# Performance work log

Hardware: AMD Instinct MI355X
Metric: run time of the kernel (lower is better)

The kernel has to match this reference:

```python
import jax, jax.numpy as jnp
import numpy as np

H = 8            # n_heads
CAP = 512        # capacity
TOPK = 2
N_HOPS = 2
ROPE_BASE = 10000.0
VOCAB = 32000
D = 512


def rope_cos_sin(T, dh, base):
    inv = 1.0 / (base ** (jnp.arange(0, dh, 2, dtype=jnp.float32) / dh))
    f = jnp.arange(T, dtype=jnp.float32)[:, None] * inv[None, :]   # [T, dh/2]
    emb = jnp.concatenate([f, f], axis=-1)                          # [T, dh]
    return jnp.cos(emb), jnp.sin(emb)


def rmsnorm(x, s):
    return x * jax.lax.rsqrt(jnp.mean(x * x, axis=-1, keepdims=True) + 1e-6) * s


def rotate_half(x):
    x1, x2 = jnp.split(x, 2, axis=-1)
    return jnp.concatenate([-x2, x1], axis=-1)


def attn_block(x, cos, sin, wqkv, wo, ln_s):
    # pre-norm causal attention with RoPE; residual included (module returns x + attn)
    C, d = x.shape
    dh = d // H
    u = rmsnorm(x, ln_s)
    qkv = u @ wqkv.T                                   # [C, 3d]
    q, k, v = [t.reshape(C, H, dh) for t in jnp.split(qkv, 3, axis=-1)]
    c = cos[:, None, :]; s = sin[:, None, :]
    q = q * c + rotate_half(q) * s
    k = k * c + rotate_half(k) * s
    scores = jnp.einsum('qhd,khd->hqk', q, k) / jnp.sqrt(jnp.float32(dh))
    causal = jnp.tril(jnp.ones((C, C), dtype=bool))
    scores = jnp.where(causal[None], scores, -1e9)
    a = jax.nn.softmax(scores, axis=-1)
    o = jnp.einsum('hqk,khd->qhd', a, v).reshape(C, d)
    return x + o @ wo.T


def ffn_block(x, w1, w2, ln_s):
    u = rmsnorm(x, ln_s)
    return x + jax.nn.gelu(u @ w1.T) @ w2.T


def hop(h, wr, attn_qkv, attn_o, attn_ln, ffn_w1, ffn_w2, ffn_ln, cos, sin):
    T, d = h.shape
    E_total = wr.shape[0]
    E = E_total - 1                                    # last expert = identity
    logits = h @ wr.T                                  # [T, E_total]
    probs = jax.nn.softmax(logits, axis=-1)
    _, idx = jax.lax.top_k(logits, TOPK)
    mask = jax.nn.one_hot(idx, E_total).sum(axis=-2) > 0     # [T, E_total]
    probs_tr = probs[:, :-1]
    mask_tr = mask[:, :-1]
    # capacity select: per-expert top-cap gated tokens -> one-hot slot [E, cap, T]
    g = jnp.where(mask_tr.T, probs_tr.T, -jnp.inf)     # [E, T]
    cap = min(CAP, T)
    _, top_idx = jax.lax.top_k(g, cap)                 # [E, cap]
    slot = jnp.zeros((E, cap, T), jnp.float32).at[
        jnp.arange(E)[:, None], jnp.arange(cap)[None, :], top_idx].set(1.0)
    slot = slot * mask_tr.T[:, None, :]
    kept = slot.sum(axis=1) > 0                        # [E, T]
    # dispatch
    xin = jnp.einsum('ect,td->ecd', slot, h)
    cos_r = jnp.einsum('ect,td->ecd', slot, cos)
    sin_r = jnp.einsum('ect,td->ecd', slot, sin)
    attn_idx = jnp.arange(0, E, 2)
    ffn_idx = jnp.arange(1, E, 2)
    out_a = jax.vmap(attn_block)(xin[attn_idx], cos_r[attn_idx], sin_r[attn_idx],
                                 attn_qkv, attn_o, attn_ln)
    out_f = jax.vmap(ffn_block)(xin[ffn_idx], ffn_w1, ffn_w2, ffn_ln)
    expert_out = jnp.zeros_like(xin).at[attn_idx].set(out_a).at[ffn_idx].set(out_f)
    # combine
    combine_w = jnp.where(kept.T, probs_tr, 0.0)       # [T, E]
    rho = combine_w.sum(axis=-1, keepdims=True)        # [T, 1]
    combine = jnp.einsum('ecd,ect,et->td', expert_out, slot, combine_w.T)
    return h + combine - rho * h


def setup_inputs() -> dict:
    key = jax.random.key(0)
    ks = jax.random.split(key, 12)
    T = 2048
    sc = 0.02
    return {
        'ids': jax.random.randint(ks[0], (T,), 0, VOCAB),
        'embed_w': jax.random.normal(ks[1], (VOCAB, D), jnp.float32) * sc,
        'router_w': jax.random.normal(ks[2], (N_HOPS, 9, D), jnp.float32) * sc,
        'attn_qkv': jax.random.normal(ks[3], (4, 3 * D, D), jnp.float32) * sc,
        'attn_o': jax.random.normal(ks[4], (4, D, D), jnp.float32) * sc,
        'attn_ln': jnp.ones((4, D), jnp.float32),
        'ffn_w1': jax.random.normal(ks[5], (4, 4 * D, D), jnp.float32) * sc,
        'ffn_w2': jax.random.normal(ks[6], (4, D, 4 * D), jnp.float32) * sc,
        'ffn_ln': jnp.ones((4, D), jnp.float32),
        'bb_qkv': jax.random.normal(ks[7], (3 * D, D), jnp.float32) * sc,
        'bb_o': jax.random.normal(ks[8], (D, D), jnp.float32) * sc,
        'bb_ln': jnp.ones((D,), jnp.float32),
        'lnout_s': jnp.ones((D,), jnp.float32),
    }


def reference(ids, embed_w, router_w, attn_qkv, attn_o, attn_ln,
              ffn_w1, ffn_w2, ffn_ln, bb_qkv, bb_o, bb_ln, lnout_s):
    T = ids.shape[0]
    dh = D // H
    h = embed_w[ids]                                   # [T, D]
    cos, sin = rope_cos_sin(T, dh, ROPE_BASE)
    h = attn_block(h, cos, sin, bb_qkv, bb_o, bb_ln)   # backbone (num_backbone=1)
    for i in range(router_w.shape[0]):                 # n_hops routed layers
        h = hop(h, router_w[i], attn_qkv, attn_o, attn_ln,
                ffn_w1, ffn_w2, ffn_ln, cos, sin)
    return rmsnorm(h, lnout_s)
```

## Files before the change

### kernel.cpp

```cpp
#include <hip/hip_runtime.h>
#include <hip/hip_bf16.h>

#define T_SEQ 2048
#define DMODEL 512
#define CEXP 512

typedef short s16x4 __attribute__((ext_vector_type(4)));
typedef short s16x8 __attribute__((ext_vector_type(8)));
typedef float f32x4 __attribute__((ext_vector_type(4)));

__device__ __forceinline__ float geluf(float x){
  float x3 = x*x*x;
  return 0.5f*x*(1.f + tanhf(0.7978845608028654f*(x + 0.044715f*x3)));
}

__device__ __forceinline__ unsigned short f2b(float x){
  unsigned int u = __float_as_uint(x);
  u += 0x7fffu + ((u >> 16) & 1u);
  return (unsigned short)(u >> 16);
}

__global__ void embed_kernel(const int* __restrict__ ids, const float* __restrict__ ew,
                             float* __restrict__ h){
  int idx = blockIdx.x*256 + threadIdx.x;
  int t = idx >> 9, d = idx & 511;
  h[idx] = ew[(size_t)ids[t]*DMODEL + d];
}

__global__ void rope_table_kernel(float* __restrict__ cosb, float* __restrict__ sinb){
  int idx = blockIdx.x*256 + threadIdx.x;
  int t = idx >> 6, i = idx & 63, j = i & 31;
  float inv = powf(10000.f, -(float)(2*j)/64.f);
  float a = (float)t * inv;
  cosb[idx] = cosf(a);
  sinb[idx] = sinf(a);
}

__global__ void rmsnorm_kernel(const float* __restrict__ in, float* __restrict__ out,
                               const float* __restrict__ scale,
                               int rows_per_group, long gstride, int scale_stride){
  int row = blockIdx.x;
  int g = row / rows_per_group, lr = row - g*rows_per_group;
  const float* x = in  + (size_t)g*gstride + (size_t)lr*DMODEL;
  float*       y = out + (size_t)g*gstride + (size_t)lr*DMODEL;
  const float* s = scale + (size_t)g*scale_stride;
  int tid = threadIdx.x;
  float ss = 0.f;
  for (int i = tid; i < DMODEL; i += 256){ float v = x[i]; ss += v*v; }
  __shared__ float red[256];
  red[tid] = ss; __syncthreads();
  for (int st = 128; st > 0; st >>= 1){ if (tid < st) red[tid] += red[tid+st]; __syncthreads(); }
  float r = rsqrtf(red[0]*(1.f/DMODEL) + 1e-6f);
  for (int i = tid; i < DMODEL; i += 256) y[i] = x[i]*r*s[i];
}

__global__ void final_rmsnorm_kernel(const float* __restrict__ in, float* __restrict__ out,
                                     const float* __restrict__ scale){
  int row = blockIdx.x;
  const float* x = in + (size_t)row*DMODEL;
  int tid = threadIdx.x;
  float ss = 0.f;
  for (int i = tid; i < DMODEL; i += 256){ float v = x[i]; ss += v*v; }
  __shared__ float red[256];
  red[tid] = ss; __syncthreads();
  for (int st = 128; st > 0; st >>= 1){ if (tid < st) red[tid] += red[tid+st]; __syncthreads(); }
  float r = rsqrtf(red[0]*(1.f/DMODEL) + 1e-6f);
  for (int i = tid; i < DMODEL; i += 256)
    out[(size_t)row*DMODEL + i] = x[i]*r*scale[i];
}

__global__ __launch_bounds__(256)
void gemm_kernel(const float* __restrict__ A, long Astride,
                 const float* __restrict__ W, long Wstride,
                 const float* __restrict__ Res, long Rstride,
                 float* __restrict__ Out, long Ostride,
                 int M, int N, int K, int act){
  int b = blockIdx.z;
  A += (size_t)b*Astride; W += (size_t)b*Wstride; Out += (size_t)b*Ostride;
  if (Res) Res += (size_t)b*Rstride;
  __shared__ float As[16][68];
  __shared__ float Ws[16][68];
  int tid = threadIdx.x;
  int tx = tid & 15, ty = tid >> 4;
  int row0 = blockIdx.x*64, col0 = blockIdx.y*64;
  float acc[4][4] = {{0.f}};
  int sm = tid >> 2;
  int skq = (tid & 3) << 2;
  int gm = row0 + sm, gn = col0 + sm;

  float4 va = make_float4(0.f,0.f,0.f,0.f);
  float4 vw = make_float4(0.f,0.f,0.f,0.f);
  if (gm < M) va = *(const float4*)&A[(size_t)gm*K + skq];
  if (gn < N) vw = *(const float4*)&W[(size_t)gn*K + skq];

  for (int k0 = 0; k0 < K; k0 += 16){
    __syncthreads();
    As[skq+0][sm] = va.x; As[skq+1][sm] = va.y; As[skq+2][sm] = va.z; As[skq+3][sm] = va.w;
    Ws[skq+0][sm] = vw.x; Ws[skq+1][sm] = vw.y; Ws[skq+2][sm] = vw.z; Ws[skq+3][sm] = vw.w;
    __syncthreads();
    if (k0 + 16 < K){
      if (gm < M) va = *(const float4*)&A[(size_t)gm*K + k0 + 16 + skq];
      if (gn < N) vw = *(const float4*)&W[(size_t)gn*K + k0 + 16 + skq];
    }
    #pragma unroll
    for (int kk = 0; kk < 16; ++kk){
      float4 av = *(const float4*)&As[kk][ty*4];
      float4 wv = *(const float4*)&Ws[kk][tx*4];
      float a[4] = {av.x, av.y, av.z, av.w};
      float w[4] = {wv.x, wv.y, wv.z, wv.w};
      #pragma unroll
      for (int i = 0; i < 4; ++i)
        #pragma unroll
        for (int j = 0; j < 4; ++j)
          acc[i][j] += a[i]*w[j];
    }
  }
  #pragma unroll
  for (int i = 0; i < 4; ++i){
    int om = row0 + ty*4 + i;
    if (om >= M) continue;
    #pragma unroll
    for (int j = 0; j < 4; ++j){
      int on = col0 + tx*4 + j;
      if (on >= N) continue;
      float v = acc[i][j];
      if (act == 1) v = geluf(v);
      if (Res) v += Res[(size_t)om*N + on];
      Out[(size_t)om*N + on] = v;
    }
  }
}

__global__ __launch_bounds__(256)
void gemm128(const float* __restrict__ A, long Astride,
             const float* __restrict__ W, long Wstride,
             const float* __restrict__ Res, long Rstride,
             float* __restrict__ Out, long Ostride,
             int M, int N, int K, int act){
  int b = blockIdx.z;
  A += (size_t)b*Astride; W += (size_t)b*Wstride; Out += (size_t)b*Ostride;
  if (Res) Res += (size_t)b*Rstride;
  __shared__ float As[16][132];
  __shared__ float Ws[16][132];
  int tid = threadIdx.x;
  int r0 = (tid >> 4) * 8;
  int c0 = (tid & 15) * 8;
  int row0 = blockIdx.x*128, col0 = blockIdx.y*128;
  int sr = tid >> 1;
  int sc = (tid & 1) * 8;
  float acc[8][8] = {{0.f}};

  float4 a0 = *(const float4*)&A[(size_t)(row0+sr)*K + sc];
  float4 a1 = *(const float4*)&A[(size_t)(row0+sr)*K + sc + 4];
  float4 w0 = *(const float4*)&W[(size_t)(col0+sr)*K + sc];
  float4 w1 = *(const float4*)&W[(size_t)(col0+sr)*K + sc + 4];

  for (int k0 = 0; k0 < K; k0 += 16){
    __syncthreads();
    As[sc+0][sr]=a0.x; As[sc+1][sr]=a0.y; As[sc+2][sr]=a0.z; As[sc+3][sr]=a0.w;
    As[sc+4][sr]=a1.x; As[sc+5][sr]=a1.y; As[sc+6][sr]=a1.z; As[sc+7][sr]=a1.w;
    Ws[sc+0][sr]=w0.x; Ws[sc+1][sr]=w0.y; Ws[sc+2][sr]=w0.z; Ws[sc+3][sr]=w0.w;
    Ws[sc+4][sr]=w1.x; Ws[sc+5][sr]=w1.y; Ws[sc+6][sr]=w1.z; Ws[sc+7][sr]=w1.w;
    __syncthreads();
    if (k0 + 16 < K){
      a0 = *(const float4*)&A[(size_t)(row0+sr)*K + k0 + 16 + sc];
      a1 = *(const float4*)&A[(size_t)(row0+sr)*K + k0 + 16 + sc + 4];
      w0 = *(const float4*)&W[(size_t)(col0+sr)*K + k0 + 16 + sc];
      w1 = *(const float4*)&W[(size_t)(col0+sr)*K + k0 + 16 + sc + 4];
    }
    #pragma unroll
    for (int kk = 0; kk < 16; ++kk){
      float a[8], w[8];
      *(float4*)&a[0] = *(const float4*)&As[kk][r0];
      *(float4*)&a[4] = *(const float4*)&As[kk][r0+4];
      *(float4*)&w[0] = *(const float4*)&Ws[kk][c0];
      *(float4*)&w[4] = *(const float4*)&Ws[kk][c0+4];
      #pragma unroll
      for (int i = 0; i < 8; ++i)
        #pragma unroll
        for (int j = 0; j < 8; ++j)
          acc[i][j] += a[i]*w[j];
    }
  }

  #pragma unroll
  for (int i = 0; i < 8; ++i){
    int gm = row0 + r0 + i;
    #pragma unroll
    for (int jj = 0; jj < 2; ++jj){
      int gn = col0 + c0 + jj*4;
      float4 v;
      v.x = acc[i][jj*4+0]; v.y = acc[i][jj*4+1];
      v.z = acc[i][jj*4+2]; v.w = acc[i][jj*4+3];
      if (act == 1){ v.x = geluf(v.x); v.y = geluf(v.y); v.z = geluf(v.z); v.w = geluf(v.w); }
      if (Res){
        float4 rv = *(const float4*)&Res[(size_t)gm*N + gn];
        v.x += rv.x; v.y += rv.y; v.z += rv.z; v.w += rv.w;
      }
      *(float4*)&Out[(size_t)gm*N + gn] = v;
    }
  }
}

__global__ __launch_bounds__(256)
void gemm_mfma(const float* __restrict__ A, long Astride,
               const float* __restrict__ W, long Wstride,
               const float* __restrict__ Res, long Rstride,
               float* __restrict__ Out, long Ostride,
               int M, int N, int K, int act){
  int b = blockIdx.z;
  A += (size_t)b*Astride; W += (size_t)b*Wstride; Out += (size_t)b*Ostride;
  if (Res) Res += (size_t)b*Rstride;

  __shared__ short As[128][40];
  __shared__ short Ws[128][40];

  int tid = threadIdx.x;
  int l = tid & 63, w = tid >> 6;
  int wrow = (w >> 1)*64, wcol = (w & 1)*64;
  int row0 = blockIdx.x*128, col0 = blockIdx.y*128;
  int lm = l & 15, lq = l >> 4;

  f32x4 acc[4][4];
  #pragma unroll
  for (int i = 0; i < 4; ++i)
    #pragma unroll
    for (int j = 0; j < 4; ++j)
      acc[i][j] = (f32x4){0.f,0.f,0.f,0.f};

  for (int k0 = 0; k0 < K; k0 += 32){
    #pragma unroll
    for (int t = 0; t < 4; ++t){
      int f4 = tid + t*256;
      int r = f4 >> 3, kq = f4 & 7;
      float4 va = *(const float4*)&A[(size_t)(row0 + r)*K + k0 + kq*4];
      s16x4 pa; pa[0]=(short)f2b(va.x); pa[1]=(short)f2b(va.y); pa[2]=(short)f2b(va.z); pa[3]=(short)f2b(va.w);
      *(s16x4*)&As[r][kq*4] = pa;
      float4 vw = *(const float4*)&W[(size_t)(col0 + r)*K + k0 + kq*4];
      s16x4 pw; pw[0]=(short)f2b(vw.x); pw[1]=(short)f2b(vw.y); pw[2]=(short)f2b(vw.z); pw[3]=(short)f2b(vw.w);
      *(s16x4*)&Ws[r][kq*4] = pw;
    }
    __syncthreads();

    s16x8 af[4], bf[4];
    #pragma unroll
    for (int rt = 0; rt < 4; ++rt)
      af[rt] = *(s16x8*)&As[wrow + rt*16 + lm][lq*8];
    #pragma unroll
    for (int ct = 0; ct < 4; ++ct)
      bf[ct] = *(s16x8*)&Ws[wcol + ct*16 + lm][lq*8];
    #pragma unroll
    for (int rt = 0; rt < 4; ++rt)
      #pragma unroll
      for (int ct = 0; ct < 4; ++ct)
        acc[rt][ct] = __builtin_amdgcn_mfma_f32_16x16x32_bf16(af[rt], bf[ct], acc[rt][ct], 0, 0, 0);
    __syncthreads();
  }

  #pragma unroll
  for (int rt = 0; rt < 4; ++rt){
    #pragma unroll
    for (int p = 0; p < 4; ++p){
      int row = row0 + wrow + rt*16 + lq*4 + p;
      #pragma unroll
      for (int ct = 0; ct < 4; ++ct){
        int col = col0 + wcol + ct*16 + lm;
        float v = acc[rt][ct][p];
        if (act == 1) v = geluf(v);
        if (Res) v += Res[(size_t)row*N + col];
        Out[(size_t)row*N + col] = v;
      }
    }
  }
}

__global__ void rope_kernel(float* __restrict__ qkv, const float* __restrict__ cosb,
                            const float* __restrict__ sinb, const int* __restrict__ map,
                            int map_gstride, int rows_per_group){
  int idx = blockIdx.x*256 + threadIdx.x;
  int row = idx >> 9;
  int rem = idx & 511;
  int sec = rem >> 8;
  int hh  = (rem >> 5) & 7;
  int j   = rem & 31;
  int t;
  if (map){
    t = map[(row/rows_per_group)*map_gstride + (row % rows_per_group)];
    if (t < 0) return;
  } else {
    t = row;
  }
  float c = cosb[t*64 + j], s = sinb[t*64 + j];
  float* p = qkv + (size_t)row*1536 + sec*512 + hh*64;
  float a = p[j], b = p[j+32];
  p[j]    = a*c - b*s;
  p[j+32] = b*c + a*s;
}

__global__ __launch_bounds__(256, 3)
void fattn_kernel(const float* __restrict__ qkv, float* __restrict__ ctx, int C){
  int tps = C >> 4;
  int pairs = tps >> 1;
  int lin = blockIdx.y * gridDim.x + blockIdx.x;
  int hh  = lin & 7;
  int bx  = lin >> 3;
  int seq = bx / pairs;
  int pr  = bx - seq*pairs;
  size_t base = (size_t)seq * C * 1536;
  const float* Qg = qkv + base + hh*64;
  const float* Kg = qkv + base + 512 + hh*64;
  const float* Vg = qkv + base + 1024 + hh*64;

  __shared__ float Qs[16][68];
  __shared__ float Ks[64][68];
  __shared__ float Ps[16][68];

  int tid = threadIdx.x;
  int tx = tid & 15, ty = tid >> 4;

  #pragma unroll 1
  for (int half = 0; half < 2; ++half){
    int lt = half ? pr : (tps - 1 - pr);
    int q0 = lt << 4;
    if (half) __syncthreads();

    *(float4*)&Qs[ty][tx*4] = *(const float4*)&Qg[(size_t)(q0 + ty)*1536 + tx*4];

    float o[4] = {0.f, 0.f, 0.f, 0.f};
    float mrow = -1e30f, lrow = 0.f;

    int nkt = (lt >> 2) + 1;
    for (int kt = 0; kt < nkt; ++kt){
      int k0 = kt << 6;
      if (kt) __syncthreads();
      for (int i = tid; i < 64*16; i += 256){
        int r = i >> 4, dq = i & 15;
        *(float4*)&Ks[r][dq*4] = *(const float4*)&Kg[(size_t)(k0 + r)*1536 + dq*4];
      }
      __syncthreads();

      const float* vbase = Vg + (size_t)k0*1536 + tx*4;
      float4 nv0 = *(const float4*)(vbase + 0*1536);
      float4 nv1 = *(const float4*)(vbase + 1*1536);
      float4 nv2 = *(const float4*)(vbase + 2*1536);
      float4 nv3 = *(const float4*)(vbase + 3*1536);

      float s[4] = {0.f, 0.f, 0.f, 0.f};
      #pragma unroll
      for (int d = 0; d < 64; d += 4){
        float4 qv = *(const float4*)&Qs[ty][d];
        float4 kv[4];
        #pragma unroll
        for (int j = 0; j < 4; ++j) kv[j] = *(const float4*)&Ks[j*16+tx][d];
        #pragma unroll
        for (int j = 0; j < 4; ++j)
          s[j] += qv.x*kv[j].x + qv.y*kv[j].y + qv.z*kv[j].z + qv.w*kv[j].w;
      }
      {
        int q = q0 + ty;
        #pragma unroll
        for (int j = 0; j < 4; ++j){
          int k = k0 + j*16 + tx;
          s[j] = (k <= q) ? s[j]*0.125f : -1e30f;
        }
      }
      {
        float m2 = fmaxf(fmaxf(s[0], s[1]), fmaxf(s[2], s[3]));
        #pragma unroll
        for (int off = 1; off < 16; off <<= 1)
          m2 = fmaxf(m2, __shfl_xor(m2, off, 64));
        float mnew = fmaxf(mrow, m2);
        float alpha = __expf(mrow - mnew);
        float p0 = __expf(s[0] - mnew);
        float p1 = __expf(s[1] - mnew);
        float p2 = __expf(s[2] - mnew);
        float p3 = __expf(s[3] - mnew);
        float rs = (p0 + p1) + (p2 + p3);
        #pragma unroll
        for (int off = 1; off < 16; off <<= 1)
          rs += __shfl_xor(rs, off, 64);
        lrow = lrow*alpha + rs;
        mrow = mnew;
        #pragma unroll
        for (int j = 0; j < 4; ++j) o[j] *= alpha;
        Ps[ty][tx]    = p0;
        Ps[ty][16+tx] = p1;
        Ps[ty][32+tx] = p2;
        Ps[ty][48+tx] = p3;
      }
      {
        #pragma unroll
        for (int kc = 0; kc < 16; ++kc){
          float4 v0 = nv0, v1 = nv1, v2 = nv2, v3 = nv3;
          if (kc < 15){
            const float* nb = vbase + (size_t)(kc+1)*4*1536;
            nv0 = *(const float4*)(nb + 0*1536);
            nv1 = *(const float4*)(nb + 1*1536);
            nv2 = *(const float4*)(nb + 2*1536);
            nv3 = *(const float4*)(nb + 3*1536);
          }
          float4 pr4 = *(const float4*)&Ps[ty][kc*4];
          o[0] += pr4.x*v0.x + pr4.y*v1.x + pr4.z*v2.x + pr4.w*v3.x;
          o[1] += pr4.x*v0.y + pr4.y*v1.y + pr4.z*v2.y + pr4.w*v3.y;
          o[2] += pr4.x*v0.z + pr4.y*v1.z + pr4.z*v2.z + pr4.w*v3.z;
          o[3] += pr4.x*v0.w + pr4.y*v1.w + pr4.z*v2.w + pr4.w*v3.w;
        }
      }
    }

    float inv = 1.f / lrow;
    float4 res;
    res.x = o[0]*inv; res.y = o[1]*inv; res.z = o[2]*inv; res.w = o[3]*inv;
    *(float4*)(ctx + (size_t)(seq*C + q0 + ty)*512 + hh*64 + tx*4) = res;
  }
}

__global__ void router_kernel(const float* __restrict__ logits, float* __restrict__ probs,
                              int* __restrict__ maskb){
  int t = blockIdx.x*256 + threadIdx.x;
  if (t >= T_SEQ) return;
  float v[9];
  float mx = -1e30f;
  for (int e = 0; e < 9; ++e){ v[e] = logits[t*9+e]; mx = fmaxf(mx, v[e]); }
  float s = 0.f;
  for (int e = 0; e < 9; ++e) s += expf(v[e]-mx);
  float inv = 1.f/s;
  for (int e = 0; e < 8; ++e) probs[t*8+e] = expf(v[e]-mx)*inv;
  int i1 = 0;
  for (int e = 1; e < 9; ++e) if (v[e] > v[i1]) i1 = e;
  int i2 = -1;
  for (int e = 0; e < 9; ++e){ if (e == i1) continue; if (i2 < 0 || v[e] > v[i2]) i2 = e; }
  maskb[t] = (1<<i1) | (1<<i2);
}

__global__ void seti_kernel(int* __restrict__ p, int v, int n){
  int i = blockIdx.x*256 + threadIdx.x;
  if (i < n) p[i] = v;
}

__global__ void rank_kernel(const float* __restrict__ probs, const int* __restrict__ maskb,
                            int* __restrict__ t2s, int* __restrict__ s2t, float* __restrict__ cw){
  int idx = blockIdx.x*256 + threadIdx.x;
  int e = idx / T_SEQ, t = idx - e*T_SEQ;
  __shared__ float spm[T_SEQ];
  int tid = threadIdx.x;
  for (int i = tid; i < T_SEQ; i += 256)
    spm[i] = ((maskb[i]>>e)&1) ? probs[i*8+e] : -1.0f;
  __syncthreads();
  int slot = -1; float w = 0.f;
  if ((maskb[t]>>e)&1){
    float p = probs[t*8+e];
    int rank = 0;
    #pragma unroll 8
    for (int t2 = 0; t2 < T_SEQ; ++t2){
      float p2 = spm[t2];
      rank += (p2 > p || (p2 == p && t2 < t)) ? 1 : 0;
    }
    if (rank < CEXP){ slot = rank; w = p; s2t[e*CEXP + rank] = t; }
  }
  t2s[t*8+e] = slot;
  cw[t*8+e] = w;
}

__global__ void gather_kernel(const float* __restrict__ h, const int* __restrict__ s2t,
                              float* __restrict__ xin){
  int idx = blockIdx.x*256 + threadIdx.x;
  int row = idx >> 9, d = idx & 511;
  int t = s2t[row];
  xin[idx] = (t >= 0) ? h[(size_t)t*DMODEL + d] : 0.f;
}

__global__ void combine_kernel(float* __restrict__ h, const float* __restrict__ eout,
                               const int* __restrict__ t2s, const float* __restrict__ cw){
  int idx = blockIdx.x*256 + threadIdx.x;
  int t = idx >> 9, d = idx & 511;
  float acc = 0.f, rho = 0.f;
  for (int e = 0; e < 8; ++e){
    int c = t2s[t*8+e];
    if (c >= 0){
      float w = cw[t*8+e];
      rho += w;
      acc += w * eout[((size_t)e*CEXP + c)*DMODEL + d];
    }
  }
  float hv = h[idx];
  h[idx] = hv + acc - rho*hv;
}

extern "C" void kernel_launch(void* const* d_in, const int* in_sizes, int n_in,
                              void* d_out, int out_size, void* d_ws, size_t ws_size,
                              hipStream_t stream){
  const int*   ids      = (const int*)  d_in[0];
  const float* embed_w  = (const float*)d_in[1];
  const float* router_w = (const float*)d_in[2];
  const float* attn_qkv = (const float*)d_in[3];
  const float* attn_o   = (const float*)d_in[4];
  const float* attn_ln  = (const float*)d_in[5];
  const float* ffn_w1   = (const float*)d_in[6];
  const float* ffn_w2   = (const float*)d_in[7];
  const float* ffn_ln   = (const float*)d_in[8];
  const float* bb_qkv   = (const float*)d_in[9];
  const float* bb_o     = (const float*)d_in[10];
  const float* bb_ln    = (const float*)d_in[11];
  const float* lnout_s  = (const float*)d_in[12];
  float* out = (float*)d_out;

  float* W    = (float*)d_ws;
  float* h    = W;
  float* cosb = h    + 1048576;
  float* sinb = cosb + 131072;
  float* xin  = sinb + 131072;
  float* u    = xin  + 2097152;
  float* big  = u    + 2097152;
  float* ctx  = big  + 4194304;
  float* eout = ctx  + 1048576;
  float* logits = eout + 2097152;
  float* probs  = logits + 18432;
  float* cw     = probs  + 16384;
  int* ibase = (int*)(cw + 16384);
  int* maskb = ibase;
  int* t2s   = maskb + 2048;
  int* s2t   = t2s   + 16384;

  embed_kernel<<<4096, 256, 0, stream>>>(ids, embed_w, h);
  rope_table_kernel<<<512, 256, 0, stream>>>(cosb, sinb);

  rmsnorm_kernel<<<2048, 256, 0, stream>>>(h, u, bb_ln, 2048, 0, 0);
  gemm128<<<dim3(16,12,1), 256, 0, stream>>>(u, 0, bb_qkv, 0, nullptr, 0, big, 0,
                                             2048, 1536, 512, 0);
  rope_kernel<<<4096, 256, 0, stream>>>(big, cosb, sinb, nullptr, 0, 2048);
  fattn_kernel<<<dim3(64,8,1), 256, 0, stream>>>(big, ctx, 2048);
  gemm_kernel<<<dim3(32,8,1), 256, 0, stream>>>(ctx, 0, bb_o, 0, h, 0, h, 0,
                                                2048, 512, 512, 0);

  for (int hop = 0; hop < 2; ++hop){
    const float* wr = router_w + (size_t)hop*9*512;
    gemm_kernel<<<dim3(32,1,1), 256, 0, stream>>>(h, 0, wr, 0, nullptr, 0, logits, 0,
                                                  2048, 9, 512, 0);
    router_kernel<<<8, 256, 0, stream>>>(logits, probs, maskb);
    seti_kernel<<<16, 256, 0, stream>>>(s2t, -1, 4096);
    rank_kernel<<<64, 256, 0, stream>>>(probs, maskb, t2s, s2t, cw);
    gather_kernel<<<8192, 256, 0, stream>>>(h, s2t, xin);

    rmsnorm_kernel<<<2048, 256, 0, stream>>>(xin,          u,          attn_ln, 512, 524288, 512);
    rmsnorm_kernel<<<2048, 256, 0, stream>>>(xin + 262144, u + 262144, ffn_ln,  512, 524288, 512);

    if (hop == 0){
      gemm128<<<dim3(4,12,4), 256, 0, stream>>>(u, 524288, attn_qkv, 786432, nullptr, 0,
                                                big, 786432, 512, 1536, 512, 0);
      rope_kernel<<<4096, 256, 0, stream>>>(big, cosb, sinb, s2t, 1024, 512);
      fattn_kernel<<<dim3(64,8,1), 256, 0, stream>>>(big, ctx, 512);
      gemm_kernel<<<dim3(8,8,4), 256, 0, stream>>>(ctx, 262144, attn_o, 262144,
                                                   xin, 524288, eout, 524288,
                                                   512, 512, 512, 0);
      gemm128<<<dim3(4,16,4), 256, 0, stream>>>(u + 262144, 524288, ffn_w1, 1048576,
                                                nullptr, 0, big, 1048576,
                                                512, 2048, 512, 1);
      gemm_kernel<<<dim3(8,8,4), 256, 0, stream>>>(big, 1048576, ffn_w2, 1048576,
                                                   xin + 262144, 524288, eout + 262144, 524288,
                                                   512, 512, 2048, 0);
    } else {
      gemm_mfma<<<dim3(4,12,4), 256, 0, stream>>>(u, 524288, attn_qkv, 786432, nullptr, 0,
                                                  big, 786432, 512, 1536, 512, 0);
      rope_kernel<<<4096, 256, 0, stream>>>(big, cosb, sinb, s2t, 1024, 512);
      fattn_kernel<<<dim3(64,8,1), 256, 0, stream>>>(big, ctx, 512);
      gemm_mfma<<<dim3(4,4,4), 256, 0, stream>>>(ctx, 262144, attn_o, 262144,
                                                 xin, 524288, eout, 524288,
                                                 512, 512, 512, 0);
      gemm_mfma<<<dim3(4,16,4), 256, 0, stream>>>(u + 262144, 524288, ffn_w1, 1048576,
                                                  nullptr, 0, big, 1048576,
                                                  512, 2048, 512, 1);
      gemm_mfma<<<dim3(4,4,4), 256, 0, stream>>>(big, 1048576, ffn_w2, 1048576,
                                                 xin + 262144, 524288, eout + 262144, 524288,
                                                 512, 512, 2048, 0);
    }

    combine_kernel<<<4096, 256, 0, stream>>>(h, eout, t2s, cw);
  }

  final_rmsnorm_kernel<<<2048, 256, 0, stream>>>(h, out, lnout_s);
}
```

Before: 1.259 ms.

## Merge attention-out and FFN-down GEMMs into one launch; double-buffer K tiles in attention

After: 2.934 ms. 133% more time.

```diff
diff --git a/kernel.cpp b/kernel.cpp
--- a/kernel.cpp
+++ b/kernel.cpp
@@ -19,6 +19,14 @@
   u += 0x7fffu + ((u >> 16) & 1u);
   return (unsigned short)(u >> 16);
 }
+
+struct GP {
+  const float* A; long As;
+  const float* W; long Ws;
+  const float* R; long Rs;
+  float* O; long Os;
+  int M, N, K, act;
+};
 
 __global__ void embed_kernel(const int* __restrict__ ids, const float* __restrict__ ew,
                              float* __restrict__ h){
@@ -69,20 +77,17 @@
     out[(size_t)row*DMODEL + i] = x[i]*r*scale[i];
 }
 
-__global__ __launch_bounds__(256)
-void gemm_kernel(const float* __restrict__ A, long Astride,
-                 const float* __restrict__ W, long Wstride,
-                 const float* __restrict__ Res, long Rstride,
-                 float* __restrict__ Out, long Ostride,
-                 int M, int N, int K, int act){
-  int b = blockIdx.z;
-  A += (size_t)b*Astride; W += (size_t)b*Wstride; Out += (size_t)b*Ostride;
-  if (Res) Res += (size_t)b*Rstride;
+__device__ __forceinline__ void gemm64_body(GP g, int bx, int by, int bz){
+  const float* A = g.A + (size_t)bz*g.As;
+  const float* W = g.W + (size_t)bz*g.Ws;
+  const float* Res = g.R ? g.R + (size_t)bz*g.Rs : nullptr;
+  float* Out = g.O + (size_t)bz*g.Os;
+  int M = g.M, N = g.N, K = g.K, act = g.act;
   __shared__ float As[16][68];
   __shared__ float Ws[16][68];
   int tid = threadIdx.x;
   int tx = tid & 15, ty = tid >> 4;
-  int row0 = blockIdx.x*64, col0 = blockIdx.y*64;
+  int row0 = bx*64, col0 = by*64;
   float acc[4][4] = {{0.f}};
   int sm = tid >> 2;
   int skq = (tid & 3) << 2;
@@ -129,6 +134,17 @@
       Out[(size_t)om*N + on] = v;
     }
   }
+}
+
+__global__ __launch_bounds__(256)
+void gemm_kernel(GP g){ gemm64_body(g, blockIdx.x, blockIdx.y, blockIdx.z); }
+
+__global__ __launch_bounds__(256)
+void gemm_dual(GP g1, GP g2, int ysplit){
+  bool first = (int)blockIdx.y < ysplit;
+  GP g = first ? g1 : g2;
+  int by = first ? blockIdx.y : blockIdx.y - ysplit;
+  gemm64_body(g, blockIdx.x, by, blockIdx.z);
 }
 
 __global__ __launch_bounds__(256)
@@ -202,15 +218,12 @@
   }
 }
 
-__global__ __launch_bounds__(256)
-void gemm_mfma(const float* __restrict__ A, long Astride,
-               const float* __restrict__ W, long Wstride,
-               const float* __restrict__ Res, long Rstride,
-               float* __restrict__ Out, long Ostride,
-               int M, int N, int K, int act){
-  int b = blockIdx.z;
-  A += (size_t)b*Astride; W += (size_t)b*Wstride; Out += (size_t)b*Ostride;
-  if (Res) Res += (size_t)b*Rstride;
+__device__ __forceinline__ void mfma_body(GP g, int bx, int by, int bz){
+  const float* A = g.A + (size_t)bz*g.As;
+  const float* W = g.W + (size_t)bz*g.Ws;
+  const float* Res = g.R ? g.R + (size_t)bz*g.Rs : nullptr;
+  float* Out = g.O + (size_t)bz*g.Os;
+  int N = g.N, K = g.K, act = g.act;
 
   __shared__ short As[128][40];
   __shared__ short Ws[128][40];
@@ -218,7 +231,7 @@
   int tid = threadIdx.x;
   int l = tid & 63, w = tid >> 6;
   int wrow = (w >> 1)*64, wcol = (w & 1)*64;
-  int row0 = blockIdx.x*128, col0 = blockIdx.y*128;
+  int row0 = bx*128, col0 = by*128;
   int lm = l & 15, lq = l >> 4;
 
   f32x4 acc[4][4];
@@ -272,6 +285,17 @@
       }
     }
   }
+}
+
+__global__ __launch_bounds__(256)
+void gemm_mfma(GP g){ mfma_body(g, blockIdx.x, blockIdx.y, blockIdx.z); }
+
+__global__ __launch_bounds__(256)
+void mfma_dual(GP g1, GP g2, int ysplit){
+  bool first = (int)blockIdx.y < ysplit;
+  GP g = first ? g1 : g2;
+  int by = first ? blockIdx.y : blockIdx.y - ysplit;
+  mfma_body(g, blockIdx.x, by, blockIdx.z);
 }
 
 __global__ void rope_kernel(float* __restrict__ qkv, const float* __restrict__ cosb,
@@ -312,11 +336,13 @@
   const float* Vg = qkv + base + 1024 + hh*64;
 
   __shared__ float Qs[16][68];
-  __shared__ float Ks[64][68];
+  __shared__ float Ks[2][64][68];
   __shared__ float Ps[16][68];
 
   int tid = threadIdx.x;
   int tx = tid & 15, ty = tid >> 4;
+  int krow = tid >> 4;
+  int kdq  = (tid & 15) * 4;
 
   #pragma unroll 1
   for (int half = 0; half < 2; ++half){
@@ -325,20 +351,25 @@
     if (half) __syncthreads();
 
     *(float4*)&Qs[ty][tx*4] = *(const float4*)&Qg[(size_t)(q0 + ty)*1536 + tx*4];
+    #pragma unroll
+    for (int t = 0; t < 4; ++t)
+      *(float4*)&Ks[0][krow + t*16][kdq] = *(const float4*)&Kg[(size_t)(krow + t*16)*1536 + kdq];
+    __syncthreads();
 
     float o[4] = {0.f, 0.f, 0.f, 0.f};
     float mrow = -1e30f, lrow = 0.f;
 
     int nkt = (lt >> 2) + 1;
     for (int kt = 0; kt < nkt; ++kt){
+      int cur = kt & 1;
       int k0 = kt << 6;
-      if (kt) __syncthreads();
-      for (int i = tid; i < 64*16; i += 256){
-        int r = i >> 4, dq = i & 15;
-        *(float4*)&Ks[r][dq*4] = *(const float4*)&Kg[(size_t)(k0 + r)*1536 + dq*4];
-      }
-      __syncthreads();
-
+      float4 kreg[4];
+      if (kt+1 < nkt){
+        int k1 = (kt+1) << 6;
+        #pragma unroll
+        for (int t = 0; t < 4; ++t)
+          kreg[t] = *(const float4*)&Kg[(size_t)(k1 + krow + t*16)*1536 + kdq];
+      }
       const float* vbase = Vg + (size_t)k0*1536 + tx*4;
       float4 nv0 = *(const float4*)(vbase + 0*1536);
       float4 nv1 = *(const float4*)(vbase + 1*1536);
@@ -351,7 +382,7 @@
         float4 qv = *(const float4*)&Qs[ty][d];
         float4 kv[4];
         #pragma unroll
-        for (int j = 0; j < 4; ++j) kv[j] = *(const float4*)&Ks[j*16+tx][d];
+        for (int j = 0; j < 4; ++j) kv[j] = *(const float4*)&Ks[cur][j*16+tx][d];
         #pragma unroll
         for (int j = 0; j < 4; ++j)
           s[j] += qv.x*kv[j].x + qv.y*kv[j].y + qv.z*kv[j].z + qv.w*kv[j].w;
@@ -405,6 +436,12 @@
           o[2] += pr4.x*v0.z + pr4.y*v1.z + pr4.z*v2.z + pr4.w*v3.z;
           o[3] += pr4.x*v0.w + pr4.y*v1.w + pr4.z*v2.w + pr4.w*v3.w;
         }
+      }
+      if (kt+1 < nkt){
+        #pragma unroll
+        for (int t = 0; t < 4; ++t)
+          *(float4*)&Ks[cur^1][krow + t*16][kdq] = kreg[t];
+        __syncthreads();
       }
     }
 
@@ -530,13 +567,13 @@
                                              2048, 1536, 512, 0);
   rope_kernel<<<4096, 256, 0, stream>>>(big, cosb, sinb, nullptr, 0, 2048);
   fattn_kernel<<<dim3(64,8,1), 256, 0, stream>>>(big, ctx, 2048);
-  gemm_kernel<<<dim3(32,8,1), 256, 0, stream>>>(ctx, 0, bb_o, 0, h, 0, h, 0,
-                                                2048, 512, 512, 0);
+  gemm_kernel<<<dim3(32,8,1), 256, 0, stream>>>(
+      GP{ctx, 0, bb_o, 0, h, 0, h, 0, 2048, 512, 512, 0});
 
   for (int hop = 0; hop < 2; ++hop){
     const float* wr = router_w + (size_t)hop*9*512;
-    gemm_kernel<<<dim3(32,1,1), 256, 0, stream>>>(h, 0, wr, 0, nullptr, 0, logits, 0,
-                                                  2048, 9, 512, 0);
+    gemm_kernel<<<dim3(32,1,1), 256, 0, stream>>>(
+        GP{h, 0, wr, 0, nullptr, 0, logits, 0, 2048, 9, 512, 0});
     router_kernel<<<8, 256, 0, stream>>>(logits, probs, maskb);
     seti_kernel<<<16, 256, 0, stream>>>(s2t, -1, 4096);
     rank_kernel<<<64, 256, 0, stream>>>(probs, maskb, t2s, s2t, cw);
@@ -550,29 +587,24 @@
                                                 big, 786432, 512, 1536, 512, 0);
       rope_kernel<<<4096, 256, 0, stream>>>(big, cosb, sinb, s2t, 1024, 512);
       fattn_kernel<<<dim3(64,8,1), 256, 0, stream>>>(big, ctx, 512);
-      gemm_kernel<<<dim3(8,8,4), 256, 0, stream>>>(ctx, 262144, attn_o, 262144,
-                                                   xin, 524288, eout, 524288,
-                                                   512, 512, 512, 0);
       gemm128<<<dim3(4,16,4), 256, 0, stream>>>(u + 262144, 524288, ffn_w1, 1048576,
                                                 nullptr, 0, big, 1048576,
                                                 512, 2048, 512, 1);
-      gemm_kernel<<<dim3(8,8,4), 256, 0, stream>>>(big, 1048576, ffn_w2, 1048576,
-                                                   xin + 262144, 524288, eout + 262144, 524288,
-                                                   512, 512, 2048, 0);
+      gemm_dual<<<dim3(8,16,4), 256, 0, stream>>>(
+          GP{ctx, 262144, attn_o, 262144, xin, 524288, eout, 524288, 512, 512, 512, 0},
+          GP{big, 1048576, ffn_w2, 1048576, xin + 262144, 524288, eout + 262144, 524288, 512, 512, 2048, 0},
+          8);
     } else {
-      gemm_mfma<<<dim3(4,12,4), 256, 0, stream>>>(u, 524288, attn_qkv, 786432, nullptr, 0,
-                                                  big, 786432, 512, 1536, 512, 0);
+      gemm_mfma<<<dim3(4,12,4), 256, 0, stream>>>(
+          GP{u, 524288, attn_qkv, 786432, nullptr, 0, big, 786432, 512, 1536, 512, 0});
       rope_kernel<<<4096, 256, 0, stream>>>(big, cosb, sinb, s2t, 1024, 512);
       fattn_kernel<<<dim3(64,8,1), 256, 0, stream>>>(big, ctx, 512);
-      gemm_mfma<<<dim3(4,4,4), 256, 0, stream>>>(ctx, 262144, attn_o, 262144,
-                                                 xin, 524288, eout, 524288,
-                                                 512, 512, 512, 0);
-      gemm_mfma<<<dim3(4,16,4), 256, 0, stream>>>(u + 262144, 524288, ffn_w1, 1048576,
-                                                  nullptr, 0, big, 1048576,
-                                                  512, 2048, 512, 1);
-      gemm_mfma<<<dim3(4,4,4), 256, 0, stream>>>(big, 1048576, ffn_w2, 1048576,
-                                                 xin + 262144, 524288, eout + 262144, 524288,
-                                                 512, 512, 2048, 0);
+      gemm_mfma<<<dim3(4,16,4), 256, 0, stream>>>(
+          GP{u + 262144, 524288, ffn_w1, 1048576, nullptr, 0, big, 1048576, 512, 2048, 512, 1});
+      mfma_dual<<<dim3(4,8,4), 256, 0, stream>>>(
+          GP{ctx, 262144, attn_o, 262144, xin, 524288, eout, 524288, 512, 512, 512, 0},
+          GP{big, 1048576, ffn_w2, 1048576, xin + 262144, 524288, eout + 262144, 524288, 512, 512, 2048, 0},
+          4);
     }
 
     combine_kernel<<<4096, 256, 0, stream>>>(h, eout, t2s, cw);
```
